# Performance work log

Measured on AMD Instinct MI355X. Metric: run time of the kernel, lower is better.

Reference implementation:

```python
import jax, jax.numpy as jnp
import numpy as np

NUM_NT = 1024
DIM = 64
B, N = 64, 4096


def setup_inputs() -> dict:
    key = jax.random.key(0)
    k1, k2 = jax.random.split(key)
    codes = jax.random.normal(k1, (B, N, DIM), dtype=jnp.float32)
    cb = jax.random.normal(k2, (NUM_NT, DIM), dtype=jnp.float32)
    # VanillaCodebook init: F.normalize -> L2-normalize each row
    codebook = cb / jnp.maximum(jnp.linalg.norm(cb, axis=-1, keepdims=True), 1e-12)
    return {"codes": codes, "codebook": codebook}


def reference(codes, codebook):
    x_sq = jnp.sum(codes * codes, axis=-1, keepdims=True)          # (B, N, 1)
    c_sq = jnp.sum(codebook * codebook, axis=-1)                   # (NT,)
    xc = jnp.einsum('bnd,kd->bnk', codes, codebook)                # (B, N, NT)
    dist2 = x_sq - 2.0 * xc + c_sq                                 # (B, N, NT)
    quant_id = jnp.argmin(dist2, axis=-1)                          # (B, N)
    quant_codes = codebook[quant_id]                               # (B, N, D)
    return quant_codes, quant_id
```

## Files before the change

### kernel.cpp

```cpp
#include <hip/hip_runtime.h>


#define NUM_NT 1024
#define DIM 64
#define M_TOTAL (64 * 4096)
#define NTILES 64
#define THR 1.0e-3f

typedef __attribute__((ext_vector_type(8))) short short8;
typedef __attribute__((ext_vector_type(4))) float f32x4;

static __device__ __forceinline__ unsigned short f2bf_rne(float f) {
    unsigned u = __builtin_bit_cast(unsigned, f);
    u += 0x7FFFu + ((u >> 16) & 1u);
    return (unsigned short)(u >> 16);
}
static __device__ __forceinline__ float bf2f(unsigned short h) {
    unsigned u = ((unsigned)h) << 16;
    return __builtin_bit_cast(float, u);
}

__global__ __launch_bounds__(64) void csq_kernel(const float* __restrict__ cb,
                                                 float* __restrict__ hcsq,
                                                 int* __restrict__ counter) {
    int k = blockIdx.x, d = threadIdx.x;
    if (k == 0 && d == 0) *counter = 0;
    float v = cb[k * DIM + d];
    float s = v * v;
    #pragma unroll
    for (int off = 32; off > 0; off >>= 1) s += __shfl_down(s, off);
    if (d == 0) hcsq[k] = 0.5f * s;
}

__global__ __launch_bounds__(256) void cb_convert(const float* __restrict__ cb,
                                                  short8* __restrict__ bh,
                                                  short8* __restrict__ bl) {
    int gtid = blockIdx.x * 256 + threadIdx.x;
    int f = gtid >> 6;
    int lane = gtid & 63;
    int t = f >> 1, kk = f & 1;
    int n = t * 16 + (lane & 15);
    int k0 = kk * 32 + 8 * (lane >> 4);
    const float* p = cb + n * DIM + k0;
    short8 h, l;
    #pragma unroll
    for (int e = 0; e < 8; ++e) {
        float v = p[e];
        unsigned short hb = f2bf_rne(v);
        h[e] = (short)hb;
        l[e] = (short)f2bf_rne(v - bf2f(hb));
    }
    bh[f * 64 + lane] = h;
    bl[f * 64 + lane] = l;
}

__global__ __launch_bounds__(256, 2) void vq_approx(const float* __restrict__ codes,
                                                    const short8* __restrict__ bh,
                                                    const short8* __restrict__ bl,
                                                    const float* __restrict__ cb,
                                                    float* __restrict__ out_codes,
                                                    float* __restrict__ out_ids,
                                                    int* __restrict__ worklist,
                                                    int* __restrict__ counter) {
    const int lane = threadIdx.x & 63;
    const int wv   = threadIdx.x >> 6;
    const int qb   = (blockIdx.x * 4 + wv) * 64;
    const int c16  = lane & 15;
    const int kg   = lane >> 4;

    short8 ah[4][2], al[4][2];
    #pragma unroll
    for (int s = 0; s < 4; ++s) {
        const float* xr = codes + (size_t)(qb + s * 16 + c16) * DIM + kg * 8;
        #pragma unroll
        for (int e = 0; e < 8; ++e) {
            float v = -xr[e];
            unsigned short hb = f2bf_rne(v);
            ah[s][0][e] = (short)hb;
            al[s][0][e] = (short)f2bf_rne(v - bf2f(hb));
            float w = -xr[32 + e];
            unsigned short hw = f2bf_rne(w);
            ah[s][1][e] = (short)hw;
            al[s][1][e] = (short)f2bf_rne(w - bf2f(hw));
        }
    }

    float d1[16], d2[16];
    int   tb[16];
    #pragma unroll
    for (int r = 0; r < 16; ++r) { d1[r] = 3.4e38f; d2[r] = 3.4e38f; tb[r] = 0; }

    short8 pvh0 = bh[0 * 64 + lane];
    short8 pvl0 = bl[0 * 64 + lane];
    short8 pvh1 = bh[1 * 64 + lane];
    short8 pvl1 = bl[1 * 64 + lane];

    for (int t = 0; t < NTILES; ++t) {
        short8 vh0 = pvh0, vl0 = pvl0, vh1 = pvh1, vl1 = pvl1;
        if (t + 1 < NTILES) {
            pvh0 = bh[(t * 2 + 2) * 64 + lane];
            pvl0 = bl[(t * 2 + 2) * 64 + lane];
            pvh1 = bh[(t * 2 + 3) * 64 + lane];
            pvl1 = bl[(t * 2 + 3) * 64 + lane];
        }
        #pragma unroll
        for (int s = 0; s < 4; ++s) {
            f32x4 acc = {0.5f, 0.5f, 0.5f, 0.5f};
            acc = __builtin_amdgcn_mfma_f32_16x16x32_bf16(ah[s][0], vh0, acc, 0, 0, 0);
            acc = __builtin_amdgcn_mfma_f32_16x16x32_bf16(al[s][0], vh0, acc, 0, 0, 0);
            acc = __builtin_amdgcn_mfma_f32_16x16x32_bf16(ah[s][0], vl0, acc, 0, 0, 0);
            acc = __builtin_amdgcn_mfma_f32_16x16x32_bf16(ah[s][1], vh1, acc, 0, 0, 0);
            acc = __builtin_amdgcn_mfma_f32_16x16x32_bf16(al[s][1], vh1, acc, 0, 0, 0);
            acc = __builtin_amdgcn_mfma_f32_16x16x32_bf16(ah[s][1], vl1, acc, 0, 0, 0);
            #pragma unroll
            for (int rr = 0; rr < 4; ++rr) {
                float d = acc[rr];
                int r = s * 4 + rr;
                bool take = d < d1[r];
                d2[r] = __builtin_amdgcn_fmed3f(d1[r], d2[r], d);
                d1[r] = fminf(d1[r], d);
                tb[r] = take ? t : tb[r];
            }
        }
    }

    const float4* cb4 = reinterpret_cast<const float4*>(cb);
    float4* oc4 = reinterpret_cast<float4*>(out_codes);
    #pragma unroll
    for (int r = 0; r < 16; ++r) {
        float dd1 = d1[r], dd2 = d2[r];
        int idv = tb[r] * 16 + c16;
        #pragma unroll
        for (int m = 1; m < 16; m <<= 1) {
            float d_o  = __shfl_xor(dd1, m, 64);
            int   i_o  = __shfl_xor(idv, m, 64);
            float d2_o = __shfl_xor(dd2, m, 64);
            float nd2 = fminf(fminf(dd2, d2_o), fmaxf(dd1, d_o));
            bool take = (d_o < dd1) || (d_o == dd1 && i_o < idv);
            dd1 = take ? d_o : dd1;
            idv = take ? i_o : idv;
            dd2 = nd2;
        }
        int q = qb + (r >> 2) * 16 + kg * 4 + (r & 3);
        oc4[(size_t)q * 16 + c16] = cb4[(size_t)idv * 16 + c16];
        if (c16 == 0) {
            out_ids[q] = (float)idv;
            if (dd2 - dd1 < THR) {
                int slot = atomicAdd(counter, 1);
                worklist[slot] = q;
            }
        }
    }
}

__global__ __launch_bounds__(256) void vq_fixup(const float* __restrict__ codes,
                                                const float* __restrict__ cb,
                                                const float* __restrict__ hcsq,
                                                const int* __restrict__ worklist,
                                                const int* __restrict__ counter,
                                                float* __restrict__ out_codes,
                                                float* __restrict__ out_ids) {
    const int lane = threadIdx.x & 63;
    const int wid  = blockIdx.x * 4 + (threadIdx.x >> 6);
    const int nw   = gridDim.x * 4;
    const int cnt  = *counter;

    for (int w = wid; w < cnt; w += nw) {
        const int q = worklist[w];
        float x[64];
        const float4* xp = reinterpret_cast<const float4*>(codes + (size_t)q * DIM);
        #pragma unroll
        for (int i = 0; i < 16; ++i) {
            float4 v = xp[i];
            x[4*i+0] = v.x; x[4*i+1] = v.y; x[4*i+2] = v.z; x[4*i+3] = v.w;
        }
        float best = 3.4e38f; int bid = 0;
        for (int jj = 0; jj < 16; ++jj) {
            int k = jj * 64 + lane;
            const float4* cp = reinterpret_cast<const float4*>(cb + (size_t)k * DIM);
            float acc = hcsq[k];
            #pragma unroll
            for (int i = 0; i < 16; ++i) {
                float4 c = cp[i];
                acc = fmaf(-x[4*i+0], c.x, acc);
                acc = fmaf(-x[4*i+1], c.y, acc);
                acc = fmaf(-x[4*i+2], c.z, acc);
                acc = fmaf(-x[4*i+3], c.w, acc);
            }
            if (acc < best) { best = acc; bid = k; }
        }
        #pragma unroll
        for (int m = 1; m < 64; m <<= 1) {
            float d_o = __shfl_xor(best, m, 64);
            int   i_o = __shfl_xor(bid, m, 64);
            bool take = (d_o < best) || (d_o == best && i_o < bid);
            best = take ? d_o : best;
            bid  = take ? i_o : bid;
        }
        int id = __shfl(bid, 0, 64);
        out_codes[(size_t)q * DIM + lane] = cb[(size_t)id * DIM + lane];
        if (lane == 0) out_ids[q] = (float)id;
    }
}

extern "C" void kernel_launch(void* const* d_in, const int* in_sizes, int n_in,
                              void* d_out, int out_size, void* d_ws, size_t ws_size,
                              hipStream_t stream) {
    const float* codes = (const float*)d_in[0];
    const float* cb    = (const float*)d_in[1];
    float* out         = (float*)d_out;

    float* out_codes = out;
    float* out_ids   = out + (size_t)M_TOTAL * DIM;

    float*  hcsq     = (float*)d_ws;
    short8* bh       = (short8*)((char*)d_ws + 4096);
    short8* bl       = (short8*)((char*)d_ws + 4096 + 128 * 1024);
    int*    counter  = (int*)((char*)d_ws + 264 * 1024);
    int*    worklist = (int*)((char*)d_ws + 268 * 1024);

    csq_kernel<<<NUM_NT, 64, 0, stream>>>(cb, hcsq, counter);
    cb_convert<<<32, 256, 0, stream>>>(cb, bh, bl);
    vq_approx<<<M_TOTAL / 256, 256, 0, stream>>>(codes, bh, bl, cb,
                                                 out_codes, out_ids,
                                                 worklist, counter);
    vq_fixup<<<512, 256, 0, stream>>>(codes, cb, hcsq, worklist, counter,
                                      out_codes, out_ids);
}
```

Measured before the change: 154.5 us.

## Switch distance GEMM from 16x16x32 to 32x32x16 bf16 MFMA tiles

Each wave now handles 32 queries against 32-codeword tiles using the 32x32x16 MFMA instead of four 16-query blocks with 16x16x32 MFMAs. The codebook split-bf16 layout is reshaped to match the new operand layout, and the argmin reduction now spans 32 lanes. The intent is fewer MFMA issues and less register traffic for A fragments per codeword tile. In exchange, each codebook fragment now serves half as many queries per wave, twice as many blocks are launched, and only half the lanes write output codes.

```diff
diff --git a/kernel.cpp b/kernel.cpp
--- a/kernel.cpp
+++ b/kernel.cpp
@@ -4,11 +4,11 @@
 #define NUM_NT 1024
 #define DIM 64
 #define M_TOTAL (64 * 4096)
-#define NTILES 64
+#define NTILES32 32
 #define THR 1.0e-3f
 
-typedef __attribute__((ext_vector_type(8))) short short8;
-typedef __attribute__((ext_vector_type(4))) float f32x4;
+typedef __attribute__((ext_vector_type(8)))  short short8;
+typedef __attribute__((ext_vector_type(16))) float f32x16;
 
 static __device__ __forceinline__ unsigned short f2bf_rne(float f) {
     unsigned u = __builtin_bit_cast(unsigned, f);
@@ -32,15 +32,15 @@
     if (d == 0) hcsq[k] = 0.5f * s;
 }
 
-__global__ __launch_bounds__(256) void cb_convert(const float* __restrict__ cb,
-                                                  short8* __restrict__ bh,
-                                                  short8* __restrict__ bl) {
+__global__ __launch_bounds__(256) void cb_convert32(const float* __restrict__ cb,
+                                                    short8* __restrict__ bh,
+                                                    short8* __restrict__ bl) {
     int gtid = blockIdx.x * 256 + threadIdx.x;
     int f = gtid >> 6;
     int lane = gtid & 63;
-    int t = f >> 1, kk = f & 1;
-    int n = t * 16 + (lane & 15);
-    int k0 = kk * 32 + 8 * (lane >> 4);
+    int t = f >> 2, ch = f & 3;
+    int n  = t * 32 + (lane & 31);
+    int k0 = ch * 16 + (lane >> 5) * 8;
     const float* p = cb + n * DIM + k0;
     short8 h, l;
     #pragma unroll
@@ -64,24 +64,22 @@
                                                     int* __restrict__ counter) {
     const int lane = threadIdx.x & 63;
     const int wv   = threadIdx.x >> 6;
-    const int qb   = (blockIdx.x * 4 + wv) * 64;
-    const int c16  = lane & 15;
-    const int kg   = lane >> 4;
-
-    short8 ah[4][2], al[4][2];
-    #pragma unroll
-    for (int s = 0; s < 4; ++s) {
-        const float* xr = codes + (size_t)(qb + s * 16 + c16) * DIM + kg * 8;
-        #pragma unroll
-        for (int e = 0; e < 8; ++e) {
-            float v = -xr[e];
-            unsigned short hb = f2bf_rne(v);
-            ah[s][0][e] = (short)hb;
-            al[s][0][e] = (short)f2bf_rne(v - bf2f(hb));
-            float w = -xr[32 + e];
-            unsigned short hw = f2bf_rne(w);
-            ah[s][1][e] = (short)hw;
-            al[s][1][e] = (short)f2bf_rne(w - bf2f(hw));
+    const int qb   = (blockIdx.x * 4 + wv) * 32;
+    const int c32  = lane & 31;
+    const int kh   = lane >> 5;
+
+    short8 ah[4], al[4];
+    {
+        const float* xr = codes + (size_t)(qb + c32) * DIM + kh * 8;
+        #pragma unroll
+        for (int ch = 0; ch < 4; ++ch) {
+            #pragma unroll
+            for (int e = 0; e < 8; ++e) {
+                float v = -xr[ch * 16 + e];
+                unsigned short hb = f2bf_rne(v);
+                ah[ch][e] = (short)hb;
+                al[ch][e] = (short)f2bf_rne(v - bf2f(hb));
+            }
         }
     }
 
@@ -90,37 +88,45 @@
     #pragma unroll
     for (int r = 0; r < 16; ++r) { d1[r] = 3.4e38f; d2[r] = 3.4e38f; tb[r] = 0; }
 
-    short8 pvh0 = bh[0 * 64 + lane];
-    short8 pvl0 = bl[0 * 64 + lane];
-    short8 pvh1 = bh[1 * 64 + lane];
-    short8 pvl1 = bl[1 * 64 + lane];
-
-    for (int t = 0; t < NTILES; ++t) {
-        short8 vh0 = pvh0, vl0 = pvl0, vh1 = pvh1, vl1 = pvl1;
-        if (t + 1 < NTILES) {
-            pvh0 = bh[(t * 2 + 2) * 64 + lane];
-            pvl0 = bl[(t * 2 + 2) * 64 + lane];
-            pvh1 = bh[(t * 2 + 3) * 64 + lane];
-            pvl1 = bl[(t * 2 + 3) * 64 + lane];
-        }
-        #pragma unroll
-        for (int s = 0; s < 4; ++s) {
-            f32x4 acc = {0.5f, 0.5f, 0.5f, 0.5f};
-            acc = __builtin_amdgcn_mfma_f32_16x16x32_bf16(ah[s][0], vh0, acc, 0, 0, 0);
-            acc = __builtin_amdgcn_mfma_f32_16x16x32_bf16(al[s][0], vh0, acc, 0, 0, 0);
-            acc = __builtin_amdgcn_mfma_f32_16x16x32_bf16(ah[s][0], vl0, acc, 0, 0, 0);
-            acc = __builtin_amdgcn_mfma_f32_16x16x32_bf16(ah[s][1], vh1, acc, 0, 0, 0);
-            acc = __builtin_amdgcn_mfma_f32_16x16x32_bf16(al[s][1], vh1, acc, 0, 0, 0);
-            acc = __builtin_amdgcn_mfma_f32_16x16x32_bf16(ah[s][1], vl1, acc, 0, 0, 0);
+    short8 pbh[4], pbl[4];
+    #pragma unroll
+    for (int ch = 0; ch < 4; ++ch) {
+        pbh[ch] = bh[ch * 64 + lane];
+        pbl[ch] = bl[ch * 64 + lane];
+    }
+
+    for (int t = 0; t < NTILES32; ++t) {
+        short8 vbh0 = pbh[0], vbh1 = pbh[1], vbh2 = pbh[2], vbh3 = pbh[3];
+        short8 vbl0 = pbl[0], vbl1 = pbl[1], vbl2 = pbl[2], vbl3 = pbl[3];
+        if (t + 1 < NTILES32) {
             #pragma unroll
-            for (int rr = 0; rr < 4; ++rr) {
-                float d = acc[rr];
-                int r = s * 4 + rr;
-                bool take = d < d1[r];
-                d2[r] = __builtin_amdgcn_fmed3f(d1[r], d2[r], d);
-                d1[r] = fminf(d1[r], d);
-                tb[r] = take ? t : tb[r];
-            }
+            for (int ch = 0; ch < 4; ++ch) {
+                pbh[ch] = bh[((t + 1) * 4 + ch) * 64 + lane];
+                pbl[ch] = bl[((t + 1) * 4 + ch) * 64 + lane];
+            }
+        }
+        f32x16 acc = {0.5f, 0.5f, 0.5f, 0.5f, 0.5f, 0.5f, 0.5f, 0.5f,
+                      0.5f, 0.5f, 0.5f, 0.5f, 0.5f, 0.5f, 0.5f, 0.5f};
+        acc = __builtin_amdgcn_mfma_f32_32x32x16_bf16(ah[0], vbh0, acc, 0, 0, 0);
+        acc = __builtin_amdgcn_mfma_f32_32x32x16_bf16(ah[1], vbh1, acc, 0, 0, 0);
+        acc = __builtin_amdgcn_mfma_f32_32x32x16_bf16(ah[2], vbh2, acc, 0, 0, 0);
+        acc = __builtin_amdgcn_mfma_f32_32x32x16_bf16(ah[3], vbh3, acc, 0, 0, 0);
+        acc = __builtin_amdgcn_mfma_f32_32x32x16_bf16(al[0], vbh0, acc, 0, 0, 0);
+        acc = __builtin_amdgcn_mfma_f32_32x32x16_bf16(al[1], vbh1, acc, 0, 0, 0);
+        acc = __builtin_amdgcn_mfma_f32_32x32x16_bf16(al[2], vbh2, acc, 0, 0, 0);
+        acc = __builtin_amdgcn_mfma_f32_32x32x16_bf16(al[3], vbh3, acc, 0, 0, 0);
+        acc = __builtin_amdgcn_mfma_f32_32x32x16_bf16(ah[0], vbl0, acc, 0, 0, 0);
+        acc = __builtin_amdgcn_mfma_f32_32x32x16_bf16(ah[1], vbl1, acc, 0, 0, 0);
+        acc = __builtin_amdgcn_mfma_f32_32x32x16_bf16(ah[2], vbl2, acc, 0, 0, 0);
+        acc = __builtin_amdgcn_mfma_f32_32x32x16_bf16(ah[3], vbl3, acc, 0, 0, 0);
+
+        #pragma unroll
+        for (int r = 0; r < 16; ++r) {
+            float d = acc[r];
+            bool take = d < d1[r];
+            d2[r] = __builtin_amdgcn_fmed3f(d1[r], d2[r], d);
+            d1[r] = fminf(d1[r], d);
+            tb[r] = take ? t : tb[r];
         }
     }
 
@@ -129,9 +135,9 @@
     #pragma unroll
     for (int r = 0; r < 16; ++r) {
         float dd1 = d1[r], dd2 = d2[r];
-        int idv = tb[r] * 16 + c16;
-        #pragma unroll
-        for (int m = 1; m < 16; m <<= 1) {
+        int idv = tb[r] * 32 + c32;
+        #pragma unroll
+        for (int m = 1; m < 32; m <<= 1) {
             float d_o  = __shfl_xor(dd1, m, 64);
             int   i_o  = __shfl_xor(idv, m, 64);
             float d2_o = __shfl_xor(dd2, m, 64);
@@ -141,9 +147,10 @@
             idv = take ? i_o : idv;
             dd2 = nd2;
         }
-        int q = qb + (r >> 2) * 16 + kg * 4 + (r & 3);
-        oc4[(size_t)q * 16 + c16] = cb4[(size_t)idv * 16 + c16];
-        if (c16 == 0) {
+        int q = qb + (r & 3) + 8 * (r >> 2) + 4 * kh;
+        if (c32 < 16)
+            oc4[(size_t)q * 16 + c32] = cb4[(size_t)idv * 16 + c32];
+        if (c32 == 0) {
             out_ids[q] = (float)idv;
             if (dd2 - dd1 < THR) {
                 int slot = atomicAdd(counter, 1);
@@ -220,8 +227,8 @@
     int*    worklist = (int*)((char*)d_ws + 268 * 1024);
 
     csq_kernel<<<NUM_NT, 64, 0, stream>>>(cb, hcsq, counter);
-    cb_convert<<<32, 256, 0, stream>>>(cb, bh, bl);
-    vq_approx<<<M_TOTAL / 256, 256, 0, stream>>>(codes, bh, bl, cb,
+    cb_convert32<<<32, 256, 0, stream>>>(cb, bh, bl);
+    vq_approx<<<M_TOTAL / 128, 256, 0, stream>>>(codes, bh, bl, cb,
                                                  out_codes, out_ids,
                                                  worklist, counter);
     vq_fixup<<<512, 256, 0, stream>>>(codes, cb, hcsq, worklist, counter,
```

Result: slower. 194.8 us (+26.1%).
